# Performance work log

Measured on AMD Instinct MI355X. Metric: run time of the kernel, lower is better.

## Reference

```python
import jax, jax.numpy as jnp
import numpy as np

B, T, D, S = 64, 512, 1024, 1024


def setup_inputs() -> dict:
    key = jax.random.key(0)
    k1, k2, k3, k4 = jax.random.split(key, 4)
    a = jax.random.normal(k1, (B, T, D), dtype=jnp.float32)
    s_prev = jax.random.normal(k2, (B, S), dtype=jnp.float32)
    # Dense(10, tanh) over concat dim D+S; Dense(1, relu). Glorot-ish scale.
    W1 = jax.random.normal(k3, (D + S, 10), dtype=jnp.float32) * (1.0 / np.sqrt(D + S))
    b1 = jnp.zeros((10,), dtype=jnp.float32)
    W2 = jax.random.normal(k4, (10, 1), dtype=jnp.float32) * (1.0 / np.sqrt(10))
    b2 = jnp.zeros((1,), dtype=jnp.float32)
    return {"a": a, "s_prev": s_prev, "W1": W1, "b1": b1, "W2": W2, "b2": b2}


def reference(a, s_prev, W1, b1, W2, b2):
    # RepeatVector: [B,S] -> [B,T,S]
    s_rep = jnp.broadcast_to(s_prev[:, None, :], (a.shape[0], a.shape[1], s_prev.shape[-1]))
    x = jnp.concatenate([a, s_rep], axis=-1)               # [B,T,D+S]
    h = jnp.tanh(jnp.einsum('btc,cu->btu', x, W1) + b1)    # [B,T,10]
    e = jax.nn.relu(jnp.einsum('btu,uo->bto', h, W2) + b2) # [B,T,1]
    attention_score = jax.nn.softmax(e, axis=1)            # softmax over time
    context_vector = jnp.sum(attention_score * a, axis=1, keepdims=True)  # [B,1,D]
    return context_vector, attention_score
```

## Files before the change

kernel.cpp:

```cpp
#include <hip/hip_runtime.h>

#define B_ 64
#define T_ 512
#define D_ 1024
#define S_ 1024
#define U_ 10

static constexpr int WS_C   = 0;
static constexpr int WS_PMZ = 640;
static constexpr int WS_E   = 1664;
static constexpr int WS_PV  = 34432;

template <int CTRL>
__device__ __forceinline__ float dpp_add(float x) {
    int yi = __builtin_amdgcn_update_dpp(0, __float_as_int(x), CTRL, 0xf, 0xf, true);
    return x + __int_as_float(yi);
}

__device__ __forceinline__ float wave_sum_uniform(float x) {
    x = dpp_add<0x111>(x);
    x = dpp_add<0x112>(x);
    x = dpp_add<0x114>(x);
    x = dpp_add<0x118>(x);
    x = dpp_add<0x142>(x);
    x = dpp_add<0x143>(x);
    return __int_as_float(__builtin_amdgcn_readlane(__float_as_int(x), 63));
}

__global__ __launch_bounds__(256) void k0_cprev(const float* __restrict__ s_prev,
                                                const float* __restrict__ W1,
                                                const float* __restrict__ b1,
                                                float* __restrict__ ws) {
    const int b = blockIdx.x;
    const int tid = threadIdx.x;

    const float4 s4 = *(const float4*)(s_prev + b * S_ + tid * 4);
    float sv[4] = {s4.x, s4.y, s4.z, s4.w};

    float acc[U_];
#pragma unroll
    for (int u = 0; u < U_; u++) acc[u] = 0.f;

    const float* wp = W1 + (size_t)(D_ + tid * 4) * U_;
#pragma unroll
    for (int q = 0; q < 10; q++) {
        float4 t = ((const float4*)wp)[q];
        float tv[4] = {t.x, t.y, t.z, t.w};
#pragma unroll
        for (int i = 0; i < 4; i++) {
            int f = q * 4 + i;
            int j = f / U_;
            int u = f % U_;
            acc[u] += sv[j] * tv[i];
        }
    }

    __shared__ float red[256][U_];
#pragma unroll
    for (int u = 0; u < U_; u++) red[tid][u] = acc[u];
    __syncthreads();
    for (int off = 128; off > 0; off >>= 1) {
        if (tid < off) {
#pragma unroll
            for (int u = 0; u < U_; u++) red[tid][u] += red[tid + off][u];
        }
        __syncthreads();
    }
    if (tid < U_) ws[WS_C + b * U_ + tid] = red[0][tid] + b1[tid];
}

__global__ __launch_bounds__(256, 2) void k1_main(const float* __restrict__ a,
                                                  const float* __restrict__ W1,
                                                  const float* __restrict__ W2,
                                                  const float* __restrict__ b2,
                                                  float* __restrict__ ws) {
    const int blk  = blockIdx.x;
    const int b    = blk >> 3;
    const int p    = blk & 7;
    const int tid  = threadIdx.x;
    const int wave = tid >> 6;
    const int lane = tid & 63;

    float w1f[4][40];
#pragma unroll
    for (int k = 0; k < 4; k++) {
        const float* wp = W1 + (size_t)(k * 256 + lane * 4) * U_;
#pragma unroll
        for (int q = 0; q < 10; q++) {
            float4 t = ((const float4*)wp)[q];
            w1f[k][q * 4 + 0] = t.x;
            w1f[k][q * 4 + 1] = t.y;
            w1f[k][q * 4 + 2] = t.z;
            w1f[k][q * 4 + 3] = t.w;
        }
    }

    float c[U_], w2v[U_];
#pragma unroll
    for (int u = 0; u < U_; u++)
        c[u] = __int_as_float(__builtin_amdgcn_readfirstlane(
                   __float_as_int(ws[WS_C + b * U_ + u])));
#pragma unroll
    for (int u = 0; u < U_; u++)
        w2v[u] = __int_as_float(__builtin_amdgcn_readfirstlane(__float_as_int(W2[u])));
    const float b2s = __int_as_float(__builtin_amdgcn_readfirstlane(__float_as_int(b2[0])));

    float v[4][4];
#pragma unroll
    for (int k = 0; k < 4; k++)
#pragma unroll
        for (int j = 0; j < 4; j++) v[k][j] = 0.f;
    float m = -1e30f, Z = 0.f;

    const int t0 = p * 64 + wave * 16;
    const float* abase = a + ((size_t)(b * T_ + t0)) * D_ + lane * 4;

    for (int tt = 0; tt < 16; tt++) {
        const float* ap = abase + (size_t)tt * D_;
        float av[4][4];
#pragma unroll
        for (int k = 0; k < 4; k++) {
            float4 t = *(const float4*)(ap + k * 256);
            av[k][0] = t.x; av[k][1] = t.y; av[k][2] = t.z; av[k][3] = t.w;
        }

        float acc[U_];
#pragma unroll
        for (int u = 0; u < U_; u++) acc[u] = 0.f;
#pragma unroll
        for (int k = 0; k < 4; k++)
#pragma unroll
            for (int j = 0; j < 4; j++)
#pragma unroll
                for (int u = 0; u < U_; u++)
                    acc[u] += av[k][j] * w1f[k][j * 10 + u];

        float e = b2s;
#pragma unroll
        for (int u = 0; u < U_; u++) {
            float s = wave_sum_uniform(acc[u]);
            float x = s + c[u];
            x = fminf(fmaxf(x, -15.f), 15.f);
            float ex = __expf(2.f * x);
            float th = 1.f - 2.f * __builtin_amdgcn_rcpf(ex + 1.f);
            e += th * w2v[u];
        }
        e = fmaxf(e, 0.f);
        if (lane == 0) ws[WS_E + b * T_ + t0 + tt] = e;

        float mn = fmaxf(m, e);
        float sc = __expf(m - mn);
        float w  = __expf(e - mn);
        Z = Z * sc + w;
#pragma unroll
        for (int k = 0; k < 4; k++)
#pragma unroll
            for (int j = 0; j < 4; j++) v[k][j] = v[k][j] * sc + w * av[k][j];
        m = mn;
    }

    __shared__ float4 vs4[4][256];
    __shared__ float  mzs[4][2];
#pragma unroll
    for (int k = 0; k < 4; k++)
        vs4[wave][k * 64 + lane] = make_float4(v[k][0], v[k][1], v[k][2], v[k][3]);
    if (lane == 0) { mzs[wave][0] = m; mzs[wave][1] = Z; }
    __syncthreads();

    float m0 = mzs[0][0], m1 = mzs[1][0], m2 = mzs[2][0], m3 = mzs[3][0];
    float mb = fmaxf(fmaxf(m0, m1), fmaxf(m2, m3));
    float f0 = __expf(m0 - mb), f1 = __expf(m1 - mb);
    float f2 = __expf(m2 - mb), f3 = __expf(m3 - mb);
    float Zb = f0 * mzs[0][1] + f1 * mzs[1][1] + f2 * mzs[2][1] + f3 * mzs[3][1];

    float4 t0v = vs4[0][tid], t1v = vs4[1][tid], t2v = vs4[2][tid], t3v = vs4[3][tid];
    float4 o;
    o.x = f0 * t0v.x + f1 * t1v.x + f2 * t2v.x + f3 * t3v.x;
    o.y = f0 * t0v.y + f1 * t1v.y + f2 * t2v.y + f3 * t3v.y;
    o.z = f0 * t0v.z + f1 * t1v.z + f2 * t2v.z + f3 * t3v.z;
    o.w = f0 * t0v.w + f1 * t1v.w + f2 * t2v.w + f3 * t3v.w;
    ((float4*)(ws + WS_PV))[blk * 256 + tid] = o;
    if (tid == 0) { ws[WS_PMZ + blk * 2] = mb; ws[WS_PMZ + blk * 2 + 1] = Zb; }
}

__global__ __launch_bounds__(256) void k2_final(const float* __restrict__ ws,
                                                float* __restrict__ out) {
    const int b = blockIdx.x;
    const int tid = threadIdx.x;

    float pm[8], pz[8];
    float mb = -1e30f;
#pragma unroll
    for (int p = 0; p < 8; p++) {
        pm[p] = ws[WS_PMZ + (b * 8 + p) * 2];
        pz[p] = ws[WS_PMZ + (b * 8 + p) * 2 + 1];
        mb = fmaxf(mb, pm[p]);
    }
    float f[8], Z = 0.f;
#pragma unroll
    for (int p = 0; p < 8; p++) { f[p] = __expf(pm[p] - mb); Z += f[p] * pz[p]; }
    const float rz = 1.f / Z;

    float4 o = make_float4(0.f, 0.f, 0.f, 0.f);
#pragma unroll
    for (int p = 0; p < 8; p++) {
        float4 t = ((const float4*)(ws + WS_PV))[(b * 8 + p) * 256 + tid];
        o.x += f[p] * t.x; o.y += f[p] * t.y; o.z += f[p] * t.z; o.w += f[p] * t.w;
    }
    o.x *= rz; o.y *= rz; o.z *= rz; o.w *= rz;
    ((float4*)out)[b * 256 + tid] = o;

    for (int t = tid; t < T_; t += 256) {
        out[B_ * D_ + b * T_ + t] = __expf(ws[WS_E + b * T_ + t] - mb) * rz;
    }
}

extern "C" void kernel_launch(void* const* d_in, const int* in_sizes, int n_in,
                              void* d_out, int out_size, void* d_ws, size_t ws_size,
                              hipStream_t stream) {
    const float* a      = (const float*)d_in[0];
    const float* s_prev = (const float*)d_in[1];
    const float* W1     = (const float*)d_in[2];
    const float* b1     = (const float*)d_in[3];
    const float* W2     = (const float*)d_in[4];
    const float* b2     = (const float*)d_in[5];
    float* out = (float*)d_out;
    float* ws  = (float*)d_ws;

    k0_cprev<<<dim3(B_), dim3(256), 0, stream>>>(s_prev, W1, b1, ws);
    k1_main<<<dim3(B_ * 8), dim3(256), 0, stream>>>(a, W1, W2, b2, ws);
    k2_final<<<dim3(B_), dim3(256), 0, stream>>>(ws, out);
}
```

Baseline: 211.2 us.

## Fuse s_prev projection into main kernel and prefetch next row of a

Removes the separate k0 kernel: each wave now computes the per-batch s_prev·W1 bias term itself with a wave reduction, which saves a launch and a global round trip. The cost is redundant work, since all 32 waves per batch repeat this 1024x10 dot product. The main time loop also double-buffers the loads of a, fetching row tt+1 while row tt is being processed, to hide memory latency. The extra registers risk spilling given the already large w1f register array and launch_bounds(256,2).

```diff
diff --git a/kernel.cpp b/kernel.cpp
--- a/kernel.cpp
+++ b/kernel.cpp
@@ -6,10 +6,9 @@
 #define S_ 1024
 #define U_ 10
 
-static constexpr int WS_C   = 0;
-static constexpr int WS_PMZ = 640;
-static constexpr int WS_E   = 1664;
-static constexpr int WS_PV  = 34432;
+static constexpr int WS_PMZ = 0;
+static constexpr int WS_E   = 1024;
+static constexpr int WS_PV  = 33792;
 
 template <int CTRL>
 __device__ __forceinline__ float dpp_add(float x) {
@@ -27,50 +26,14 @@
     return __int_as_float(__builtin_amdgcn_readlane(__float_as_int(x), 63));
 }
 
-__global__ __launch_bounds__(256) void k0_cprev(const float* __restrict__ s_prev,
-                                                const float* __restrict__ W1,
-                                                const float* __restrict__ b1,
-                                                float* __restrict__ ws) {
-    const int b = blockIdx.x;
-    const int tid = threadIdx.x;
-
-    const float4 s4 = *(const float4*)(s_prev + b * S_ + tid * 4);
-    float sv[4] = {s4.x, s4.y, s4.z, s4.w};
-
-    float acc[U_];
-#pragma unroll
-    for (int u = 0; u < U_; u++) acc[u] = 0.f;
-
-    const float* wp = W1 + (size_t)(D_ + tid * 4) * U_;
-#pragma unroll
-    for (int q = 0; q < 10; q++) {
-        float4 t = ((const float4*)wp)[q];
-        float tv[4] = {t.x, t.y, t.z, t.w};
-#pragma unroll
-        for (int i = 0; i < 4; i++) {
-            int f = q * 4 + i;
-            int j = f / U_;
-            int u = f % U_;
-            acc[u] += sv[j] * tv[i];
-        }
-    }
-
-    __shared__ float red[256][U_];
-#pragma unroll
-    for (int u = 0; u < U_; u++) red[tid][u] = acc[u];
-    __syncthreads();
-    for (int off = 128; off > 0; off >>= 1) {
-        if (tid < off) {
-#pragma unroll
-            for (int u = 0; u < U_; u++) red[tid][u] += red[tid + off][u];
-        }
-        __syncthreads();
-    }
-    if (tid < U_) ws[WS_C + b * U_ + tid] = red[0][tid] + b1[tid];
+__device__ __forceinline__ float uload(const float* p) {
+    return __int_as_float(__builtin_amdgcn_readfirstlane(__float_as_int(*p)));
 }
 
 __global__ __launch_bounds__(256, 2) void k1_main(const float* __restrict__ a,
+                                                  const float* __restrict__ s_prev,
                                                   const float* __restrict__ W1,
+                                                  const float* __restrict__ b1,
                                                   const float* __restrict__ W2,
                                                   const float* __restrict__ b2,
                                                   float* __restrict__ ws) {
@@ -81,6 +44,37 @@
     const int wave = tid >> 6;
     const int lane = tid & 63;
 
+    float c[U_];
+    {
+        float cacc[U_];
+#pragma unroll
+        for (int u = 0; u < U_; u++) cacc[u] = 0.f;
+#pragma unroll
+        for (int r = 0; r < 4; r++) {
+            const float4 s4 = *(const float4*)(s_prev + b * S_ + r * 256 + lane * 4);
+            const float svv[4] = {s4.x, s4.y, s4.z, s4.w};
+#pragma unroll
+            for (int i = 0; i < 4; i++) {
+                const int s = r * 256 + lane * 4 + i;
+                const float* wp = W1 + (size_t)(D_ + s) * U_;
+#pragma unroll
+                for (int h = 0; h < 5; h++) {
+                    float2 t = ((const float2*)wp)[h];
+                    cacc[2 * h]     += svv[i] * t.x;
+                    cacc[2 * h + 1] += svv[i] * t.y;
+                }
+            }
+        }
+#pragma unroll
+        for (int u = 0; u < U_; u++)
+            c[u] = wave_sum_uniform(cacc[u]) + uload(b1 + u);
+    }
+
+    float w2v[U_];
+#pragma unroll
+    for (int u = 0; u < U_; u++) w2v[u] = uload(W2 + u);
+    const float b2s = uload(b2);
+
     float w1f[4][40];
 #pragma unroll
     for (int k = 0; k < 4; k++) {
@@ -95,16 +89,6 @@
         }
     }
 
-    float c[U_], w2v[U_];
-#pragma unroll
-    for (int u = 0; u < U_; u++)
-        c[u] = __int_as_float(__builtin_amdgcn_readfirstlane(
-                   __float_as_int(ws[WS_C + b * U_ + u])));
-#pragma unroll
-    for (int u = 0; u < U_; u++)
-        w2v[u] = __int_as_float(__builtin_amdgcn_readfirstlane(__float_as_int(W2[u])));
-    const float b2s = __int_as_float(__builtin_amdgcn_readfirstlane(__float_as_int(b2[0])));
-
     float v[4][4];
 #pragma unroll
     for (int k = 0; k < 4; k++)
@@ -115,13 +99,23 @@
     const int t0 = p * 64 + wave * 16;
     const float* abase = a + ((size_t)(b * T_ + t0)) * D_ + lane * 4;
 
+    float4 cur[4], nxt[4];
+#pragma unroll
+    for (int k = 0; k < 4; k++) cur[k] = *(const float4*)(abase + k * 256);
+
+#pragma unroll 2
     for (int tt = 0; tt < 16; tt++) {
-        const float* ap = abase + (size_t)tt * D_;
+        if (tt < 15) {
+            const float* apn = abase + (size_t)(tt + 1) * D_;
+#pragma unroll
+            for (int k = 0; k < 4; k++) nxt[k] = *(const float4*)(apn + k * 256);
+        }
+
         float av[4][4];
 #pragma unroll
         for (int k = 0; k < 4; k++) {
-            float4 t = *(const float4*)(ap + k * 256);
-            av[k][0] = t.x; av[k][1] = t.y; av[k][2] = t.z; av[k][3] = t.w;
+            av[k][0] = cur[k].x; av[k][1] = cur[k].y;
+            av[k][2] = cur[k].z; av[k][3] = cur[k].w;
         }
 
         float acc[U_];
@@ -157,6 +151,9 @@
 #pragma unroll
             for (int j = 0; j < 4; j++) v[k][j] = v[k][j] * sc + w * av[k][j];
         m = mn;
+
+#pragma unroll
+        for (int k = 0; k < 4; k++) cur[k] = nxt[k];
     }
 
     __shared__ float4 vs4[4][256];
@@ -227,7 +224,6 @@
     float* out = (float*)d_out;
     float* ws  = (float*)d_ws;
 
-    k0_cprev<<<dim3(B_), dim3(256), 0, stream>>>(s_prev, W1, b1, ws);
-    k1_main<<<dim3(B_ * 8), dim3(256), 0, stream>>>(a, W1, W2, b2, ws);
+    k1_main<<<dim3(B_ * 8), dim3(256), 0, stream>>>(a, s_prev, W1, b1, W2, b2, ws);
     k2_final<<<dim3(B_), dim3(256), 0, stream>>>(ws, out);
 }
```

Measured after the change: 209.6 us. No clear change (-0.8%).
